# Performance work log

Hardware: AMD Instinct MI355X
Metric: run time of the kernel (lower is better)

## Reference

```python
import jax, jax.numpy as jnp
import numpy as np

HEADS = 8
C = 256            # in_channels == out_channels
NUM_STAR = 4
G = 32             # num graphs
N = 100000         # num nodes
LN_EPS = 1e-5


def setup_inputs() -> dict:
    key = jax.random.key(0)
    ks = jax.random.split(key, 9)
    stars = jax.random.normal(ks[0], (G, NUM_STAR, C), jnp.float32)
    nodes = jax.random.normal(ks[1], (N, C), jnp.float32)
    batch = jnp.sort(jax.random.randint(ks[2], (N,), 0, G))
    s = 1.0 / np.sqrt(C).astype(np.float32)
    Wq_w = jax.random.normal(ks[3], (C, C), jnp.float32) * s
    Wk_w = jax.random.normal(ks[4], (C, C), jnp.float32) * s
    Wv_w = jax.random.normal(ks[5], (C, C), jnp.float32) * s
    Wq_b = jnp.zeros((C,), jnp.float32)
    Wk_b = jnp.zeros((C,), jnp.float32)
    Wv_b = jnp.zeros((C,), jnp.float32)
    ln_gamma = jnp.ones((C,), jnp.float32)
    ln_beta = jnp.zeros((C,), jnp.float32)
    return dict(stars=stars, nodes=nodes, batch=batch,
                Wq_w=Wq_w, Wq_b=Wq_b, Wk_w=Wk_w, Wk_b=Wk_b,
                Wv_w=Wv_w, Wv_b=Wv_b, ln_gamma=ln_gamma, ln_beta=ln_beta)


def reference(stars, nodes, batch, Wq_w, Wq_b, Wk_w, Wk_b, Wv_w, Wv_b, ln_gamma, ln_beta):
    g, num_star, c = stars.shape
    n = nodes.shape[0]
    h = HEADS
    dh = c // h
    s_total = g * num_star                       # number of star nodes
    num_seg = n + s_total

    # x = [nodes; flattened stars]  (star index of (graph gidx, star i) = n + num_star*gidx + i)
    x = jnp.concatenate([nodes, stars.reshape(-1, c)], axis=0)     # [n+S, c]
    q = (x @ Wq_w.T + Wq_b).reshape(-1, h, dh)
    k = (x @ Wk_w.T + Wk_b).reshape(-1, h, dh)
    v = (x @ Wv_w.T + Wv_b).reshape(-1, h, dh)

    # edges: every node -> each of its graph's stars, plus star self-loops (use_star=True)
    rows = (n + num_star * batch[None, :] + jnp.arange(num_star)[:, None]).reshape(-1)  # [num_star*n]
    cols = jnp.broadcast_to(jnp.arange(n), (num_star, n)).reshape(-1)
    star_idx = jnp.arange(n, n + s_total)
    ei = jnp.concatenate([rows, star_idx])       # targets (query side)
    ej = jnp.concatenate([cols, star_idx])       # sources (key/value side)

    qe = q[ei]                                   # [E, h, dh]
    ke = k[ej]
    ve = v[ej]

    score = jnp.einsum('ehd,ehd->eh', qe, ke) / np.sqrt(dh).astype(np.float32)

    # segment softmax over target index (PyG-style, +1e-16 in denominator)
    m = jax.ops.segment_max(score, ei, num_segments=num_seg)
    m = jnp.where(jnp.isfinite(m), m, 0.0)       # empty segments -> 0
    ex = jnp.exp(score - m[ei])
    denom = jax.ops.segment_sum(ex, ei, num_segments=num_seg)
    coef = ex / (denom[ei] + 1e-16)              # [E, h]

    # dropout is identity in eval mode
    out = jax.ops.segment_sum(ve * coef[:, :, None], ei, num_segments=num_seg)  # [n+S, h, dh]
    new_stars = out[n:].reshape(g, num_star, c)

    new_stars = jax.nn.elu(new_stars)            # activation
    new_stars = new_stars + stars                # residual

    mu = jnp.mean(new_stars, axis=-1, keepdims=True)
    var = jnp.mean(jnp.square(new_stars - mu), axis=-1, keepdims=True)
    new_stars = (new_stars - mu) / jnp.sqrt(var + LN_EPS) * ln_gamma + ln_beta
    return new_stars
```

## Files before the change

### kernel.cpp

```cpp
#include <hip/hip_runtime.h>
#include <math.h>

#define HEADS 8
#define C 256
#define NUM_STAR 4
#define SLOTS 32
#define RSQRT_DH 0.17677669529663688f
#define LN_EPS 1e-5f
#define PF 16
#define CWK 16
#define RND 64
#define XB 264
#define ST 40
#define CNP (C * ST)
#define EP 40

typedef __attribute__((ext_vector_type(8))) short short8;
typedef __attribute__((ext_vector_type(4))) float floatx4;

__device__ __forceinline__ unsigned int f2b(float f) {
    unsigned int u = __float_as_uint(f);
    return (u + 0x7fffu + ((u >> 16) & 1u)) >> 16;
}
__device__ __forceinline__ unsigned int pk_bf16(float lo, float hi) {
    unsigned int r;
    asm("v_cvt_pk_bf16_f32 %0, %1, %2" : "=v"(r) : "v"(lo), "v"(hi));
    return r;
}
__device__ __forceinline__ float fcomp(const float4& v, int jj) {
    return jj == 0 ? v.x : jj == 1 ? v.y : jj == 2 ? v.z : v.w;
}

__device__ __forceinline__ void block_sync_lds() {
    asm volatile("s_waitcnt lgkmcnt(0)" ::: "memory");
    __builtin_amdgcn_sched_barrier(0);
    __builtin_amdgcn_s_barrier();
    __builtin_amdgcn_sched_barrier(0);
}

__global__ void k_star_prep(const float* __restrict__ stars,
                            const float* __restrict__ Wq_w, const float* __restrict__ Wq_b,
                            const float* __restrict__ Wk_w, const float* __restrict__ Wk_b,
                            unsigned short* __restrict__ U16, float* __restrict__ eself,
                            float* __restrict__ denom,
                            const int* __restrict__ batch, int N, int G,
                            int* __restrict__ gstart) {
    if (blockIdx.x == gridDim.x - 1) {
        int g = threadIdx.x;
        if (g > G) return;
        if (g == 0) { gstart[0] = 0; return; }
        if (g == G) { gstart[G] = N; return; }
        int lo = 0, hi = N;
        while (lo < hi) {
            int mid = (lo + hi) >> 1;
            if (batch[mid] < g) lo = mid + 1; else hi = mid;
        }
        gstart[g] = lo;
        return;
    }

    __shared__ float xs[C];
    __shared__ float qv[C];
    __shared__ float kv[C];
    const int gs = blockIdx.x;
    const int g = gs >> 2, s = gs & 3;
    const int t = threadIdx.x;

    xs[t] = stars[gs * C + t];
    __syncthreads();

    float aq = Wq_b[t], ak = Wk_b[t];
    const float* wq = Wq_w + (size_t)t * C;
    const float* wk = Wk_w + (size_t)t * C;
    #pragma unroll 4
    for (int j = 0; j < C; j += 4) {
        float4 x4 = *(const float4*)(xs + j);
        float4 a4 = *(const float4*)(wq + j);
        aq += a4.x * x4.x + a4.y * x4.y + a4.z * x4.z + a4.w * x4.w;
        float4 b4 = *(const float4*)(wk + j);
        ak += b4.x * x4.x + b4.y * x4.y + b4.z * x4.z + b4.w * x4.w;
    }
    qv[t] = aq; kv[t] = ak;
    __syncthreads();

    {
        float p = qv[t] * kv[t];
        #pragma unroll
        for (int off = 16; off; off >>= 1) p += __shfl_down(p, off, 32);
        if ((t & 31) == 0) {
            int h = t >> 5;
            float e = __expf(p * RSQRT_DH);
            eself[g * SLOTS + s * HEADS + h] = e;
            denom[g * SLOTS + s * HEADS + h] = e;
        }
    }

    {
        const int c = t;
        #pragma unroll
        for (int h = 0; h < HEADS; ++h) {
            float u = 0.f;
            for (int d = 0; d < 32; ++d)
                u += Wk_w[(size_t)(h * 32 + d) * C + c] * qv[h * 32 + d];
            U16[((size_t)g * SLOTS + s * HEADS + h) * C + c] =
                (unsigned short)f2b(u * RSQRT_DH);
        }
    }
}

__global__ __launch_bounds__(256, 2)
void k_fused(const float* __restrict__ nodes, const unsigned short* __restrict__ U16,
             const int* __restrict__ gstart, float* __restrict__ denom,
             float* __restrict__ Ypart) {
    __shared__ unsigned short x_nc[4 * CWK * XB];
    __shared__ unsigned short x_cn[2 * CNP];
    __shared__ unsigned short e_lds[2 * SLOTS * EP];

    const int g = blockIdx.x / PF, pb = blockIdx.x % PF;
    const int t = threadIdx.x;
    const int wv = t >> 6;
    const int l  = t & 63;
    const int lr = l & 15;
    const int q  = l >> 4;

    const int glo = gstart[g], ghi = gstart[g + 1];
    const int len = ghi - glo;
    const int L = (len + PF - 1) / PF;
    const int lo = glo + pb * L;
    const int hi = min(lo + L, ghi);
    const int nr = (hi > lo) ? (hi - lo + RND - 1) / RND : 0;

    short8 ureg[2][8];
    {
        const unsigned short* ug = U16 + (size_t)g * SLOTS * C;
        #pragma unroll
        for (int st2 = 0; st2 < 2; ++st2)
            #pragma unroll
            for (int kt = 0; kt < 8; ++kt)
                ureg[st2][kt] = *(const short8*)&ug[(st2 * 16 + lr) * C + q * 8 + kt * 32];
    }

    const floatx4 z4 = {0.f, 0.f, 0.f, 0.f};
    floatx4 yacc[2][4];
    #pragma unroll
    for (int a = 0; a < 2; ++a)
        #pragma unroll
        for (int b = 0; b < 4; ++b) yacc[a][b] = z4;
    float dsum[8];
    #pragma unroll
    for (int i = 0; i < 8; ++i) dsum[i] = 0.f;

    unsigned short* xw = &x_nc[wv * CWK * XB];
    const int p_own = wv >> 1, hw = wv & 1;

    float4 xr[CWK];
    if (nr > 0) {
        int base = lo + wv * CWK;
        #pragma unroll
        for (int i = 0; i < CWK; ++i) {
            int gn = base + i;
            xr[i] = (gn < hi) ? *(const float4*)&nodes[(size_t)gn * C + l * 4]
                              : make_float4(0.f, 0.f, 0.f, 0.f);
        }
    }

    for (int rd = 0; rd < nr; ++rd) {
        block_sync_lds();

        #pragma unroll
        for (int i = 0; i < CWK; ++i) {
            uint2 w2;
            w2.x = pk_bf16(xr[i].x, xr[i].y);
            w2.y = pk_bf16(xr[i].z, xr[i].w);
            *(uint2*)&xw[i * XB + l * 4] = w2;
        }
        #pragma unroll
        for (int jj = 0; jj < 4; ++jj) {
            const int c = 4 * l + jj;
            const int sz = ((c >> 2) ^ (c >> 4)) & 3;
            uint4 ulo, uhi;
            ulo.x = pk_bf16(fcomp(xr[0], jj), fcomp(xr[1], jj));
            ulo.y = pk_bf16(fcomp(xr[2], jj), fcomp(xr[3], jj));
            ulo.z = pk_bf16(fcomp(xr[4], jj), fcomp(xr[5], jj));
            ulo.w = pk_bf16(fcomp(xr[6], jj), fcomp(xr[7], jj));
            uhi.x = pk_bf16(fcomp(xr[8], jj), fcomp(xr[9], jj));
            uhi.y = pk_bf16(fcomp(xr[10], jj), fcomp(xr[11], jj));
            uhi.z = pk_bf16(fcomp(xr[12], jj), fcomp(xr[13], jj));
            uhi.w = pk_bf16(fcomp(xr[14], jj), fcomp(xr[15], jj));
            unsigned short* basep = &x_cn[p_own * CNP + c * ST];
            *(uint4*)&basep[((hw * 2 + 0) ^ sz) * 8] = ulo;
            *(uint4*)&basep[((hw * 2 + 1) ^ sz) * 8] = uhi;
        }
        if (rd + 1 < nr) {
            int base = lo + (rd + 1) * RND + wv * CWK;
            #pragma unroll
            for (int i = 0; i < CWK; ++i) {
                int gn = base + i;
                xr[i] = (gn < hi) ? *(const float4*)&nodes[(size_t)gn * C + l * 4]
                                  : make_float4(0.f, 0.f, 0.f, 0.f);
            }
        }

        floatx4 sacc0 = z4, sacc1 = z4;
        {
            const unsigned short* xrw = &xw[lr * XB + q * 8];
            #pragma unroll
            for (int kt = 0; kt < 8; ++kt) {
                short8 bx = *(const short8*)(xrw + kt * 32);
                sacc0 = __builtin_amdgcn_mfma_f32_16x16x32_bf16(ureg[0][kt], bx, sacc0, 0, 0, 0);
                sacc1 = __builtin_amdgcn_mfma_f32_16x16x32_bf16(ureg[1][kt], bx, sacc1, 0, 0, 0);
            }
        }

        {
            int base = lo + rd * RND + wv * CWK;
            const bool valid = (base + lr) < hi;
            unsigned short* ew = &e_lds[p_own * SLOTS * EP + hw * 16 + lr];
            #pragma unroll
            for (int r = 0; r < 4; ++r) {
                float e0 = valid ? __expf(sacc0[r]) : 0.f;
                float e1 = valid ? __expf(sacc1[r]) : 0.f;
                dsum[r]     += e0;
                dsum[4 + r] += e1;
                ew[(q * 4 + r) * EP]      = (unsigned short)f2b(e0);
                ew[(16 + q * 4 + r) * EP] = (unsigned short)f2b(e1);
            }
        }
        block_sync_lds();

        #pragma unroll
        for (int p = 0; p < 2; ++p) {
            short8 pa0 = *(const short8*)&e_lds[(p * SLOTS + lr) * EP + q * 8];
            short8 pa1 = *(const short8*)&e_lds[(p * SLOTS + 16 + lr) * EP + q * 8];
            #pragma unroll
            for (int ct = 0; ct < 4; ++ct) {
                const int c = wv * 64 + ct * 16 + lr;
                const int sz = ((c >> 2) ^ (c >> 4)) & 3;
                short8 bx = *(const short8*)&x_cn[p * CNP + c * ST + ((q ^ sz) * 8)];
                yacc[0][ct] = __builtin_amdgcn_mfma_f32_16x16x32_bf16(pa0, bx, yacc[0][ct], 0, 0, 0);
                yacc[1][ct] = __builtin_amdgcn_mfma_f32_16x16x32_bf16(pa1, bx, yacc[1][ct], 0, 0, 0);
            }
        }
    }

    {
        float* yg = &Ypart[(((size_t)g * PF + pb) * SLOTS) * C];
        #pragma unroll
        for (int st = 0; st < 2; ++st)
            #pragma unroll
            for (int ct = 0; ct < 4; ++ct)
                #pragma unroll
                for (int r = 0; r < 4; ++r)
                    yg[(st * 16 + q * 4 + r) * C + wv * 64 + ct * 16 + lr] = yacc[st][ct][r];
    }

    #pragma unroll
    for (int i = 0; i < 8; ++i) {
        float v = dsum[i];
        v += __shfl_xor(v, 1);
        v += __shfl_xor(v, 2);
        v += __shfl_xor(v, 4);
        v += __shfl_xor(v, 8);
        dsum[i] = v;
    }
    if (lr == 0 && nr > 0) {
        #pragma unroll
        for (int mt = 0; mt < 2; ++mt)
            #pragma unroll
            for (int r = 0; r < 4; ++r)
                atomicAdd(&denom[g * SLOTS + mt * 16 + q * 4 + r], dsum[mt * 4 + r]);
    }
}

__global__ void k_epilogue(const float* __restrict__ stars,
                           const float* __restrict__ Wv_w, const float* __restrict__ Wv_b,
                           const float* __restrict__ gamma, const float* __restrict__ beta,
                           const float* __restrict__ Ypart, const float* __restrict__ eself,
                           const float* __restrict__ denom, float* __restrict__ out) {
    __shared__ float xs[C];
    __shared__ float yl[HEADS * C];
    __shared__ float cs[HEADS], ivd[HEADS], scl[HEADS];
    __shared__ float rb[8];

    const int gs = blockIdx.x;
    const int g = gs >> 2, s = gs & 3;
    const int t = threadIdx.x;

    xs[t] = stars[gs * C + t];
    if (t < HEADS) {
        float dn = denom[g * SLOTS + s * HEADS + t];
        float iv = 1.f / (dn + 1e-16f);
        ivd[t] = iv;
        cs[t] = eself[g * SLOTS + s * HEADS + t] * iv;
        scl[t] = dn * iv;
    }
    __syncthreads();

    for (int i = t; i < HEADS * C; i += 256) {
        int h = i >> 8, j = i & 255;
        float sum = 0.f;
        #pragma unroll
        for (int pbi = 0; pbi < PF; ++pbi)
            sum += Ypart[(((size_t)g * PF + pbi) * SLOTS + s * HEADS + h) * C + j];
        yl[i] = sum * ivd[h] + cs[h] * xs[j];
    }
    __syncthreads();

    const int c = t, h = c >> 5;
    float a = 0.f;
    const float* wv = Wv_w + (size_t)c * C;
    const float* yh = &yl[h * C];
    #pragma unroll 4
    for (int j = 0; j < C; j += 4) {
        float4 w4 = *(const float4*)(wv + j);
        float4 y4 = *(const float4*)(yh + j);
        a += w4.x * y4.x + w4.y * y4.y + w4.z * y4.z + w4.w * y4.w;
    }
    a += Wv_b[c] * scl[h];

    float v = a > 0.f ? a : (__expf(a) - 1.f);
    float r = v + xs[c];

    float ssum = r;
    #pragma unroll
    for (int off = 32; off; off >>= 1) ssum += __shfl_down(ssum, off, 64);
    const int wid = t >> 6, lane = t & 63;
    if (lane == 0) rb[wid] = ssum;
    __syncthreads();
    const float mu = (rb[0] + rb[1] + rb[2] + rb[3]) * (1.f / 256.f);
    const float d = r - mu;
    float vsum = d * d;
    #pragma unroll
    for (int off = 32; off; off >>= 1) vsum += __shfl_down(vsum, off, 64);
    if (lane == 0) rb[4 + wid] = vsum;
    __syncthreads();
    const float var = (rb[4] + rb[5] + rb[6] + rb[7]) * (1.f / 256.f);
    out[gs * C + c] = d * rsqrtf(var + LN_EPS) * gamma[c] + beta[c];
}

extern "C" void kernel_launch(void* const* d_in, const int* in_sizes, int n_in,
                              void* d_out, int out_size, void* d_ws, size_t ws_size,
                              hipStream_t stream) {
    const float* stars = (const float*)d_in[0];
    const float* nodes = (const float*)d_in[1];
    const int*   batch = (const int*)d_in[2];
    const float* Wq_w  = (const float*)d_in[3];
    const float* Wq_b  = (const float*)d_in[4];
    const float* Wk_w  = (const float*)d_in[5];
    const float* Wk_b  = (const float*)d_in[6];
    const float* Wv_w  = (const float*)d_in[7];
    const float* Wv_b  = (const float*)d_in[8];
    const float* gamma = (const float*)d_in[9];
    const float* beta  = (const float*)d_in[10];

    const int N = in_sizes[1] / C;
    const int G = in_sizes[0] / (NUM_STAR * C);

    unsigned short* U16 = (unsigned short*)d_ws;
    float* eself = (float*)((char*)d_ws + (size_t)G * SLOTS * C * 2);
    float* denom = eself + (size_t)G * SLOTS;
    float* Ypart = denom + (size_t)G * SLOTS;
    int*   gstart = (int*)(Ypart + (size_t)G * PF * SLOTS * C);

    float* out = (float*)d_out;

    k_star_prep<<<G * NUM_STAR + 1, 256, 0, stream>>>(stars, Wq_w, Wq_b, Wk_w, Wk_b,
                                                      U16, eself, denom,
                                                      batch, N, G, gstart);
    k_fused<<<G * PF, 256, 0, stream>>>(nodes, U16, gstart, denom, Ypart);
    k_epilogue<<<G * NUM_STAR, 256, 0, stream>>>(stars, Wv_w, Wv_b, gamma, beta,
                                                 Ypart, eself, denom, out);
}
```

Before: 70.65 us.

## Halve per-round node tile, raise occupancy and partition count, swizzle LDS

Each round now processes 32 nodes (8 per wave) instead of 64, which shrinks the register prefetch buffer and the LDS footprint. That allows three blocks per CU, and the node range is split into 24 partitions per graph instead of 16. The three LDS arrays are merged into one buffer with new XOR swizzles for the row-major and column-major node copies, and the exp-score tile is written only for the 8 valid rows. The score MFMA still runs 16 rows per wave, so half of it is wasted work, and the larger partition count enlarges the partial-output writes and the later reduction.

Result: slower. 83.72 us (+18.5%).

```diff
diff --git a/kernel.cpp b/kernel.cpp
--- a/kernel.cpp
+++ b/kernel.cpp
@@ -7,13 +7,17 @@
 #define SLOTS 32
 #define RSQRT_DH 0.17677669529663688f
 #define LN_EPS 1e-5f
-#define PF 16
-#define CWK 16
-#define RND 64
+#define PF 24
+#define CWK 8
+#define RND 32
 #define XB 264
 #define ST 40
-#define CNP (C * ST)
 #define EP 40
+
+#define X_NC 0
+#define X_CN 8448
+#define E_OFF 18688
+#define LDS_TOT 19968
 
 typedef __attribute__((ext_vector_type(8))) short short8;
 typedef __attribute__((ext_vector_type(4))) float floatx4;
@@ -30,7 +34,6 @@
 __device__ __forceinline__ float fcomp(const float4& v, int jj) {
     return jj == 0 ? v.x : jj == 1 ? v.y : jj == 2 ? v.z : v.w;
 }
-
 __device__ __forceinline__ void block_sync_lds() {
     asm volatile("s_waitcnt lgkmcnt(0)" ::: "memory");
     __builtin_amdgcn_sched_barrier(0);
@@ -108,13 +111,11 @@
     }
 }
 
-__global__ __launch_bounds__(256, 2)
+__global__ __launch_bounds__(256, 3)
 void k_fused(const float* __restrict__ nodes, const unsigned short* __restrict__ U16,
              const int* __restrict__ gstart, float* __restrict__ denom,
              float* __restrict__ Ypart) {
-    __shared__ unsigned short x_nc[4 * CWK * XB];
-    __shared__ unsigned short x_cn[2 * CNP];
-    __shared__ unsigned short e_lds[2 * SLOTS * EP];
+    __shared__ unsigned short lds[LDS_TOT];
 
     const int g = blockIdx.x / PF, pb = blockIdx.x % PF;
     const int t = threadIdx.x;
@@ -150,9 +151,6 @@
     #pragma unroll
     for (int i = 0; i < 8; ++i) dsum[i] = 0.f;
 
-    unsigned short* xw = &x_nc[wv * CWK * XB];
-    const int p_own = wv >> 1, hw = wv & 1;
-
     float4 xr[CWK];
     if (nr > 0) {
         int base = lo + wv * CWK;
@@ -169,27 +167,24 @@
 
         #pragma unroll
         for (int i = 0; i < CWK; ++i) {
+            const int row = wv * CWK + i;
             uint2 w2;
             w2.x = pk_bf16(xr[i].x, xr[i].y);
             w2.y = pk_bf16(xr[i].z, xr[i].w);
-            *(uint2*)&xw[i * XB + l * 4] = w2;
+            const int off = row * XB + (l >> 3) * 32
+                          + ((((l >> 1) & 3) ^ (row & 3)) * 8) + (l & 1) * 4;
+            *(uint2*)&lds[X_NC + off] = w2;
         }
         #pragma unroll
         for (int jj = 0; jj < 4; ++jj) {
             const int c = 4 * l + jj;
-            const int sz = ((c >> 2) ^ (c >> 4)) & 3;
-            uint4 ulo, uhi;
-            ulo.x = pk_bf16(fcomp(xr[0], jj), fcomp(xr[1], jj));
-            ulo.y = pk_bf16(fcomp(xr[2], jj), fcomp(xr[3], jj));
-            ulo.z = pk_bf16(fcomp(xr[4], jj), fcomp(xr[5], jj));
-            ulo.w = pk_bf16(fcomp(xr[6], jj), fcomp(xr[7], jj));
-            uhi.x = pk_bf16(fcomp(xr[8], jj), fcomp(xr[9], jj));
-            uhi.y = pk_bf16(fcomp(xr[10], jj), fcomp(xr[11], jj));
-            uhi.z = pk_bf16(fcomp(xr[12], jj), fcomp(xr[13], jj));
-            uhi.w = pk_bf16(fcomp(xr[14], jj), fcomp(xr[15], jj));
-            unsigned short* basep = &x_cn[p_own * CNP + c * ST];
-            *(uint4*)&basep[((hw * 2 + 0) ^ sz) * 8] = ulo;
-            *(uint4*)&basep[((hw * 2 + 1) ^ sz) * 8] = uhi;
+            const int slot = wv ^ ((c >> 3) & 3);
+            uint4 u4;
+            u4.x = pk_bf16(fcomp(xr[0], jj), fcomp(xr[1], jj));
+            u4.y = pk_bf16(fcomp(xr[2], jj), fcomp(xr[3], jj));
+            u4.z = pk_bf16(fcomp(xr[4], jj), fcomp(xr[5], jj));
+            u4.w = pk_bf16(fcomp(xr[6], jj), fcomp(xr[7], jj));
+            *(uint4*)&lds[X_CN + c * ST + slot * 8] = u4;
         }
         if (rd + 1 < nr) {
             int base = lo + (rd + 1) * RND + wv * CWK;
@@ -203,40 +198,45 @@
 
         floatx4 sacc0 = z4, sacc1 = z4;
         {
-            const unsigned short* xrw = &xw[lr * XB + q * 8];
+            const int row = wv * CWK + lr;
+            const int rb = row * XB + ((q ^ (row & 3)) * 8);
             #pragma unroll
             for (int kt = 0; kt < 8; ++kt) {
-                short8 bx = *(const short8*)(xrw + kt * 32);
+                short8 bx = *(const short8*)&lds[X_NC + rb + kt * 32];
                 sacc0 = __builtin_amdgcn_mfma_f32_16x16x32_bf16(ureg[0][kt], bx, sacc0, 0, 0, 0);
                 sacc1 = __builtin_amdgcn_mfma_f32_16x16x32_bf16(ureg[1][kt], bx, sacc1, 0, 0, 0);
             }
         }
 
         {
-            int base = lo + rd * RND + wv * CWK;
-            const bool valid = (base + lr) < hi;
-            unsigned short* ew = &e_lds[p_own * SLOTS * EP + hw * 16 + lr];
+            const int rbase = lo + rd * RND;
+            const bool valid = (lr < 8) && (rbase + wv * CWK + lr < hi);
+            const int ncol = wv * CWK + (lr & 7);
             #pragma unroll
             for (int r = 0; r < 4; ++r) {
                 float e0 = valid ? __expf(sacc0[r]) : 0.f;
                 float e1 = valid ? __expf(sacc1[r]) : 0.f;
                 dsum[r]     += e0;
                 dsum[4 + r] += e1;
-                ew[(q * 4 + r) * EP]      = (unsigned short)f2b(e0);
-                ew[(16 + q * 4 + r) * EP] = (unsigned short)f2b(e1);
+                if (valid) {
+                    lds[E_OFF + (q * 4 + r) * EP + ncol]      = (unsigned short)f2b(e0);
+                    lds[E_OFF + (16 + q * 4 + r) * EP + ncol] = (unsigned short)f2b(e1);
+                } else if (lr < 8) {
+                    lds[E_OFF + (q * 4 + r) * EP + ncol]      = 0;
+                    lds[E_OFF + (16 + q * 4 + r) * EP + ncol] = 0;
+                }
             }
         }
         block_sync_lds();
 
-        #pragma unroll
-        for (int p = 0; p < 2; ++p) {
-            short8 pa0 = *(const short8*)&e_lds[(p * SLOTS + lr) * EP + q * 8];
-            short8 pa1 = *(const short8*)&e_lds[(p * SLOTS + 16 + lr) * EP + q * 8];
+        {
+            short8 pa0 = *(const short8*)&lds[E_OFF + lr * EP + q * 8];
+            short8 pa1 = *(const short8*)&lds[E_OFF + (16 + lr) * EP + q * 8];
             #pragma unroll
             for (int ct = 0; ct < 4; ++ct) {
                 const int c = wv * 64 + ct * 16 + lr;
-                const int sz = ((c >> 2) ^ (c >> 4)) & 3;
-                short8 bx = *(const short8*)&x_cn[p * CNP + c * ST + ((q ^ sz) * 8)];
+                const int slot = q ^ ((c >> 3) & 3);
+                short8 bx = *(const short8*)&lds[X_CN + c * ST + slot * 8];
                 yacc[0][ct] = __builtin_amdgcn_mfma_f32_16x16x32_bf16(pa0, bx, yacc[0][ct], 0, 0, 0);
                 yacc[1][ct] = __builtin_amdgcn_mfma_f32_16x16x32_bf16(pa1, bx, yacc[1][ct], 0, 0, 0);
             }
```

## Give each wave its own node range and reduce partial outputs through LDS

Applied to the files above, without the earlier changes.

Drops the block-wide barriers from the main loop. Each wave now processes a private contiguous node range with wave-local LDS staging, and accumulates the full 32x256 output tile in registers. The four wave partials are summed through LDS once at the end before a single coalesced store. The price is much higher register pressure (128 accumulator floats per lane), a second MFMA with half its K dimension zero-padded, and scalar strided LDS gathers to build the transposed operand. It also fully unrolls the Wk projection loop in the star-prep kernel.

Measured after the change: 95.23 us. +34.8%, slower.

```diff
diff --git a/kernel.cpp b/kernel.cpp
--- a/kernel.cpp
+++ b/kernel.cpp
@@ -8,12 +8,15 @@
 #define RSQRT_DH 0.17677669529663688f
 #define LN_EPS 1e-5f
 #define PF 16
-#define CWK 16
-#define RND 64
-#define XB 264
-#define ST 40
-#define CNP (C * ST)
-#define EP 40
+#define WN 16
+#define XB2 260
+#define EP2 40
+
+#define XNC_W (WN * XB2)
+#define E_W   (SLOTS * EP2)
+#define E_OFF (4 * XNC_W)
+#define LDS_USH (E_OFF + 4 * E_W)
+#define YLP 260
 
 typedef __attribute__((ext_vector_type(8))) short short8;
 typedef __attribute__((ext_vector_type(4))) float floatx4;
@@ -26,16 +29,6 @@
     unsigned int r;
     asm("v_cvt_pk_bf16_f32 %0, %1, %2" : "=v"(r) : "v"(lo), "v"(hi));
     return r;
-}
-__device__ __forceinline__ float fcomp(const float4& v, int jj) {
-    return jj == 0 ? v.x : jj == 1 ? v.y : jj == 2 ? v.z : v.w;
-}
-
-__device__ __forceinline__ void block_sync_lds() {
-    asm volatile("s_waitcnt lgkmcnt(0)" ::: "memory");
-    __builtin_amdgcn_sched_barrier(0);
-    __builtin_amdgcn_s_barrier();
-    __builtin_amdgcn_sched_barrier(0);
 }
 
 __global__ void k_star_prep(const float* __restrict__ stars,
@@ -100,6 +93,7 @@
         #pragma unroll
         for (int h = 0; h < HEADS; ++h) {
             float u = 0.f;
+            #pragma unroll
             for (int d = 0; d < 32; ++d)
                 u += Wk_w[(size_t)(h * 32 + d) * C + c] * qv[h * 32 + d];
             U16[((size_t)g * SLOTS + s * HEADS + h) * C + c] =
@@ -112,9 +106,7 @@
 void k_fused(const float* __restrict__ nodes, const unsigned short* __restrict__ U16,
              const int* __restrict__ gstart, float* __restrict__ denom,
              float* __restrict__ Ypart) {
-    __shared__ unsigned short x_nc[4 * CWK * XB];
-    __shared__ unsigned short x_cn[2 * CNP];
-    __shared__ unsigned short e_lds[2 * SLOTS * EP];
+    __shared__ unsigned short lds[LDS_USH];
 
     const int g = blockIdx.x / PF, pb = blockIdx.x % PF;
     const int t = threadIdx.x;
@@ -125,150 +117,158 @@
 
     const int glo = gstart[g], ghi = gstart[g + 1];
     const int len = ghi - glo;
-    const int L = (len + PF - 1) / PF;
-    const int lo = glo + pb * L;
-    const int hi = min(lo + L, ghi);
-    const int nr = (hi > lo) ? (hi - lo + RND - 1) / RND : 0;
-
-    short8 ureg[2][8];
-    {
-        const unsigned short* ug = U16 + (size_t)g * SLOTS * C;
-        #pragma unroll
-        for (int st2 = 0; st2 < 2; ++st2)
-            #pragma unroll
-            for (int kt = 0; kt < 8; ++kt)
-                ureg[st2][kt] = *(const short8*)&ug[(st2 * 16 + lr) * C + q * 8 + kt * 32];
-    }
+    const int Lb = (len + PF - 1) / PF;
+    const int blo = glo + pb * Lb;
+    const int bhi = min(blo + Lb, ghi);
+    const int blen = max(bhi - blo, 0);
+    const int wlen = (blen + 3) >> 2;
+    const int wlo = blo + wv * wlen;
+    const int whi = min(wlo + wlen, bhi);
+    const int nrw = (whi > wlo) ? (whi - wlo + WN - 1) / WN : 0;
+
+    unsigned short* xnc = &lds[wv * XNC_W];
+    unsigned short* el  = &lds[E_OFF + wv * E_W];
 
     const floatx4 z4 = {0.f, 0.f, 0.f, 0.f};
-    floatx4 yacc[2][4];
+    floatx4 yacc[2][16];
     #pragma unroll
     for (int a = 0; a < 2; ++a)
         #pragma unroll
-        for (int b = 0; b < 4; ++b) yacc[a][b] = z4;
+        for (int b = 0; b < 16; ++b) yacc[a][b] = z4;
     float dsum[8];
     #pragma unroll
     for (int i = 0; i < 8; ++i) dsum[i] = 0.f;
 
-    unsigned short* xw = &x_nc[wv * CWK * XB];
-    const int p_own = wv >> 1, hw = wv & 1;
-
-    float4 xr[CWK];
-    if (nr > 0) {
-        int base = lo + wv * CWK;
-        #pragma unroll
-        for (int i = 0; i < CWK; ++i) {
-            int gn = base + i;
-            xr[i] = (gn < hi) ? *(const float4*)&nodes[(size_t)gn * C + l * 4]
-                              : make_float4(0.f, 0.f, 0.f, 0.f);
-        }
-    }
-
-    for (int rd = 0; rd < nr; ++rd) {
-        block_sync_lds();
-
-        #pragma unroll
-        for (int i = 0; i < CWK; ++i) {
-            uint2 w2;
-            w2.x = pk_bf16(xr[i].x, xr[i].y);
-            w2.y = pk_bf16(xr[i].z, xr[i].w);
-            *(uint2*)&xw[i * XB + l * 4] = w2;
-        }
-        #pragma unroll
-        for (int jj = 0; jj < 4; ++jj) {
-            const int c = 4 * l + jj;
-            const int sz = ((c >> 2) ^ (c >> 4)) & 3;
-            uint4 ulo, uhi;
-            ulo.x = pk_bf16(fcomp(xr[0], jj), fcomp(xr[1], jj));
-            ulo.y = pk_bf16(fcomp(xr[2], jj), fcomp(xr[3], jj));
-            ulo.z = pk_bf16(fcomp(xr[4], jj), fcomp(xr[5], jj));
-            ulo.w = pk_bf16(fcomp(xr[6], jj), fcomp(xr[7], jj));
-            uhi.x = pk_bf16(fcomp(xr[8], jj), fcomp(xr[9], jj));
-            uhi.y = pk_bf16(fcomp(xr[10], jj), fcomp(xr[11], jj));
-            uhi.z = pk_bf16(fcomp(xr[12], jj), fcomp(xr[13], jj));
-            uhi.w = pk_bf16(fcomp(xr[14], jj), fcomp(xr[15], jj));
-            unsigned short* basep = &x_cn[p_own * CNP + c * ST];
-            *(uint4*)&basep[((hw * 2 + 0) ^ sz) * 8] = ulo;
-            *(uint4*)&basep[((hw * 2 + 1) ^ sz) * 8] = uhi;
-        }
-        if (rd + 1 < nr) {
-            int base = lo + (rd + 1) * RND + wv * CWK;
-            #pragma unroll
-            for (int i = 0; i < CWK; ++i) {
-                int gn = base + i;
-                xr[i] = (gn < hi) ? *(const float4*)&nodes[(size_t)gn * C + l * 4]
-                                  : make_float4(0.f, 0.f, 0.f, 0.f);
-            }
-        }
-
-        floatx4 sacc0 = z4, sacc1 = z4;
+    if (nrw > 0) {
         {
-            const unsigned short* xrw = &xw[lr * XB + q * 8];
-            #pragma unroll
-            for (int kt = 0; kt < 8; ++kt) {
-                short8 bx = *(const short8*)(xrw + kt * 32);
-                sacc0 = __builtin_amdgcn_mfma_f32_16x16x32_bf16(ureg[0][kt], bx, sacc0, 0, 0, 0);
-                sacc1 = __builtin_amdgcn_mfma_f32_16x16x32_bf16(ureg[1][kt], bx, sacc1, 0, 0, 0);
-            }
-        }
-
+            const int slot = l >> 1, half = l & 1;
+            *(uint4*)&el[slot * EP2 + 16 + half * 8] = make_uint4(0, 0, 0, 0);
+        }
+        short8 ureg[2][8];
         {
-            int base = lo + rd * RND + wv * CWK;
-            const bool valid = (base + lr) < hi;
-            unsigned short* ew = &e_lds[p_own * SLOTS * EP + hw * 16 + lr];
-            #pragma unroll
-            for (int r = 0; r < 4; ++r) {
-                float e0 = valid ? __expf(sacc0[r]) : 0.f;
-                float e1 = valid ? __expf(sacc1[r]) : 0.f;
-                dsum[r]     += e0;
-                dsum[4 + r] += e1;
-                ew[(q * 4 + r) * EP]      = (unsigned short)f2b(e0);
-                ew[(16 + q * 4 + r) * EP] = (unsigned short)f2b(e1);
-            }
-        }
-        block_sync_lds();
-
-        #pragma unroll
-        for (int p = 0; p < 2; ++p) {
-            short8 pa0 = *(const short8*)&e_lds[(p * SLOTS + lr) * EP + q * 8];
-            short8 pa1 = *(const short8*)&e_lds[(p * SLOTS + 16 + lr) * EP + q * 8];
-            #pragma unroll
-            for (int ct = 0; ct < 4; ++ct) {
-                const int c = wv * 64 + ct * 16 + lr;
-                const int sz = ((c >> 2) ^ (c >> 4)) & 3;
-                short8 bx = *(const short8*)&x_cn[p * CNP + c * ST + ((q ^ sz) * 8)];
-                yacc[0][ct] = __builtin_amdgcn_mfma_f32_16x16x32_bf16(pa0, bx, yacc[0][ct], 0, 0, 0);
-                yacc[1][ct] = __builtin_amdgcn_mfma_f32_16x16x32_bf16(pa1, bx, yacc[1][ct], 0, 0, 0);
-            }
-        }
-    }
-
+            const unsigned short* ug = U16 + (size_t)g * SLOTS * C;
+            #pragma unroll
+            for (int st2 = 0; st2 < 2; ++st2)
+                #pragma unroll
+                for (int kt = 0; kt < 8; ++kt)
+                    ureg[st2][kt] = *(const short8*)&ug[(st2 * 16 + lr) * C + q * 8 + kt * 32];
+        }
+
+        float4 xr[WN];
+        {
+            #pragma unroll
+            for (int i = 0; i < WN; ++i) {
+                int gn = wlo + i;
+                if (gn >= whi) gn = wlo;
+                xr[i] = *(const float4*)&nodes[(size_t)gn * C + l * 4];
+            }
+        }
+
+        for (int rd = 0; rd < nrw; ++rd) {
+            #pragma unroll
+            for (int i = 0; i < WN; ++i) {
+                uint2 w2;
+                w2.x = pk_bf16(xr[i].x, xr[i].y);
+                w2.y = pk_bf16(xr[i].z, xr[i].w);
+                *(uint2*)&xnc[i * XB2 + 4 * l] = w2;
+            }
+            if (rd + 1 < nrw) {
+                #pragma unroll
+                for (int i = 0; i < WN; ++i) {
+                    int gn = wlo + (rd + 1) * WN + i;
+                    if (gn >= whi) gn = wlo;
+                    xr[i] = *(const float4*)&nodes[(size_t)gn * C + l * 4];
+                }
+            }
+
+            floatx4 s0 = z4, s1 = z4;
+            {
+                const unsigned short* xrw = &xnc[lr * XB2 + q * 8];
+                #pragma unroll
+                for (int kt = 0; kt < 8; ++kt) {
+                    short8 bx = *(const short8*)(xrw + kt * 32);
+                    s0 = __builtin_amdgcn_mfma_f32_16x16x32_bf16(ureg[0][kt], bx, s0, 0, 0, 0);
+                    s1 = __builtin_amdgcn_mfma_f32_16x16x32_bf16(ureg[1][kt], bx, s1, 0, 0, 0);
+                }
+            }
+
+            {
+                const bool valid = (wlo + rd * WN + lr) < whi;
+                #pragma unroll
+                for (int r = 0; r < 4; ++r) {
+                    float e0 = valid ? __expf(s0[r]) : 0.f;
+                    float e1 = valid ? __expf(s1[r]) : 0.f;
+                    dsum[r]     += e0;
+                    dsum[4 + r] += e1;
+                    el[(q * 4 + r) * EP2 + lr]        = (unsigned short)f2b(e0);
+                    el[(16 + q * 4 + r) * EP2 + lr]   = (unsigned short)f2b(e1);
+                }
+            }
+
+            {
+                short8 pa0 = *(const short8*)&el[lr * EP2 + q * 8];
+                short8 pa1 = *(const short8*)&el[(16 + lr) * EP2 + q * 8];
+                #pragma unroll
+                for (int ct = 0; ct < 16; ++ct) {
+                    short8 bx;
+                    if (q < 2) {
+                        const unsigned short* col = &xnc[q * 8 * XB2 + ct * 16 + lr];
+                        #pragma unroll
+                        for (int j = 0; j < 8; ++j) bx[j] = (short)col[j * XB2];
+                    } else {
+                        #pragma unroll
+                        for (int j = 0; j < 8; ++j) bx[j] = 0;
+                    }
+                    yacc[0][ct] = __builtin_amdgcn_mfma_f32_16x16x32_bf16(pa0, bx, yacc[0][ct], 0, 0, 0);
+                    yacc[1][ct] = __builtin_amdgcn_mfma_f32_16x16x32_bf16(pa1, bx, yacc[1][ct], 0, 0, 0);
+                }
+            }
+        }
+
+        #pragma unroll
+        for (int i = 0; i < 8; ++i) {
+            float v = dsum[i];
+            v += __shfl_xor(v, 1);
+            v += __shfl_xor(v, 2);
+            v += __shfl_xor(v, 4);
+            v += __shfl_xor(v, 8);
+            dsum[i] = v;
+        }
+        if (lr == 0) {
+            #pragma unroll
+            for (int st2 = 0; st2 < 2; ++st2)
+                #pragma unroll
+                for (int r = 0; r < 4; ++r)
+                    atomicAdd(&denom[g * SLOTS + st2 * 16 + q * 4 + r], dsum[st2 * 4 + r]);
+        }
+    }
+
+    float* Yl = (float*)lds;
+    __syncthreads();
+    #pragma unroll
+    for (int w = 0; w < 4; ++w) {
+        if (wv == w) {
+            #pragma unroll
+            for (int st2 = 0; st2 < 2; ++st2)
+                #pragma unroll
+                for (int ct = 0; ct < 16; ++ct)
+                    #pragma unroll
+                    for (int r = 0; r < 4; ++r) {
+                        int idx = (st2 * 16 + q * 4 + r) * YLP + ct * 16 + lr;
+                        if (w == 0) Yl[idx] = yacc[st2][ct][r];
+                        else        Yl[idx] += yacc[st2][ct][r];
+                    }
+        }
+        __syncthreads();
+    }
     {
         float* yg = &Ypart[(((size_t)g * PF + pb) * SLOTS) * C];
         #pragma unroll
-        for (int st = 0; st < 2; ++st)
-            #pragma unroll
-            for (int ct = 0; ct < 4; ++ct)
-                #pragma unroll
-                for (int r = 0; r < 4; ++r)
-                    yg[(st * 16 + q * 4 + r) * C + wv * 64 + ct * 16 + lr] = yacc[st][ct][r];
-    }
-
-    #pragma unroll
-    for (int i = 0; i < 8; ++i) {
-        float v = dsum[i];
-        v += __shfl_xor(v, 1);
-        v += __shfl_xor(v, 2);
-        v += __shfl_xor(v, 4);
-        v += __shfl_xor(v, 8);
-        dsum[i] = v;
-    }
-    if (lr == 0 && nr > 0) {
-        #pragma unroll
-        for (int mt = 0; mt < 2; ++mt)
-            #pragma unroll
-            for (int r = 0; r < 4; ++r)
-                atomicAdd(&denom[g * SLOTS + mt * 16 + q * 4 + r], dsum[mt * 4 + r]);
+        for (int k = 0; k < 8; ++k) {
+            int flat = k * 1024 + t * 4;
+            int row = flat >> 8, col = flat & 255;
+            *(float4*)&yg[flat] = *(const float4*)&Yl[row * YLP + col];
+        }
     }
 }
 
```
